# Optimization experiments

Hardware: AMD Instinct MI355X
Metric: run time of the kernel (lower is better)

Reference implementation:

```python
import jax, jax.numpy as jnp
import numpy as np

K = 5        # kernel_size per dim
DIM = 3      # pseudo-coordinate dim
KTOT = K ** DIM   # 125 kernel weight matrices
S = 2 ** DIM      # 8 basis products for degree-1 open B-spline
KNN = 3


def spline_basis(ea):
    """Degree-1 open B-spline basis. ea: [E, DIM] in [0,1).
    Returns basis [E, S] and kernel weight indices wi [E, S]."""
    v = ea * (K - 1)
    b = jnp.floor(v)
    f = v - b                      # fractional part, grads flow here
    bi = b.astype(jnp.int32)
    bases, idxs = [], []
    for c in range(S):             # static loop over 2^DIM corner combos
        bs = jnp.ones(ea.shape[0], ea.dtype)
        wi = jnp.zeros(ea.shape[0], jnp.int32)
        for d in range(DIM):
            bit = (c >> d) & 1
            bs = bs * (f[:, d] if bit else 1.0 - f[:, d])
            wi = wi + jnp.clip(bi[:, d] + bit, 0, K - 1) * (K ** d)
        bases.append(bs)
        idxs.append(wi)
    return jnp.stack(bases, 1), jnp.stack(idxs, 1)


def spline_conv(x, src, dst, basis, wi, W, Wroot, bias):
    """SplineConv with aggr='mean', root weight and bias (PyG defaults)."""
    N, Cin = x.shape
    E = src.shape[0]
    xs = x[src]                                   # [E, Cin] gather
    vals = xs[:, None, :] * basis[:, :, None]     # [E, S, Cin]
    seg = (dst[:, None] * KTOT + wi).reshape(-1)  # bucket by (dst node, kernel)
    A = jax.ops.segment_sum(vals.reshape(-1, Cin), seg,
                            num_segments=N * KTOT).reshape(N, KTOT, Cin)
    out = jnp.einsum('nki,kio->no', A, W)         # apply kernel bank once
    deg = jax.ops.segment_sum(jnp.ones(E, x.dtype), dst, num_segments=N)
    out = out / jnp.maximum(deg, 1.0)[:, None]    # mean aggregation
    return out + x @ Wroot + bias


def knn_interpolate(x, pos_x, pos_y, batch_x, batch_y, k):
    """PyG knn_interpolate: inverse-squared-distance weighted k-NN average."""
    off = 1e5  # separate batches in coordinate space
    px = pos_x + batch_x[:, None].astype(pos_x.dtype) * off
    py = pos_y + batch_y[:, None].astype(pos_y.dtype) * off
    d2 = (jnp.sum(py ** 2, 1)[:, None] + jnp.sum(px ** 2, 1)[None, :]
          - 2.0 * (py @ px.T))                    # [Ny, Nx]
    negd, idx = jax.lax.top_k(-d2, k)             # k nearest
    w = 1.0 / jnp.maximum(-negd, 1e-16)           # [Ny, k]
    return (w[:, :, None] * x[idx]).sum(1) / w.sum(1)[:, None]


def setup_inputs() -> dict:
    key = jax.random.key(0)
    ks = jax.random.split(key, 12)
    N, E, Ny, C = 8192, 131072, 16384, 64
    return {
        'x': jax.random.normal(ks[0], (N, C), jnp.float32),
        'edge_index': jax.random.randint(ks[1], (2, E), 0, N, jnp.int32),
        'edge_attr': jax.random.uniform(ks[2], (E, DIM), jnp.float32),
        'pos_x': jax.random.normal(ks[3], (N, 3), jnp.float32),
        'batch_x': jnp.zeros((N,), jnp.int32),
        'pos_y': jax.random.normal(ks[4], (Ny, 3), jnp.float32),
        'batch_y': jnp.zeros((Ny,), jnp.int32),
        'Wa': jax.random.normal(ks[5], (KTOT, C, C), jnp.float32) * 0.05,
        'roota': jax.random.normal(ks[6], (C, C), jnp.float32) * 0.05,
        'biasa': jnp.zeros((C,), jnp.float32),
        'Wb': jax.random.normal(ks[7], (KTOT, C, C), jnp.float32) * 0.05,
        'rootb': jax.random.normal(ks[8], (C, C), jnp.float32) * 0.05,
        'biasb': jnp.zeros((C,), jnp.float32),
    }


def reference(x, edge_index, edge_attr, pos_x, batch_x, pos_y, batch_y,
              Wa, roota, biasa, Wb, rootb, biasb):
    src, dst = edge_index[0], edge_index[1]
    basis, wi = spline_basis(edge_attr)
    h = jax.nn.elu(spline_conv(x, src, dst, basis, wi, Wa, roota, biasa))
    h = jax.nn.elu(spline_conv(h, src, dst, basis, wi, Wb, rootb, biasb))
    return knn_interpolate(h, pos_x, pos_y, batch_x, batch_y, KNN)
```

## Files before the change

### kernel.cpp

```cpp
#include <hip/hip_runtime.h>
#include <hip/hip_bf16.h>
#include <math.h>

#define CDIV(a,b) (((a)+(b)-1)/(b))
#define WPCV 8
#define KCH 32

typedef __attribute__((ext_vector_type(8))) short bf16x8;
typedef __attribute__((ext_vector_type(4))) float f32x4;

__device__ __forceinline__ float elu_f(float x){ return x > 0.f ? x : expm1f(x); }
__device__ __forceinline__ unsigned short f2bf(float x){
    __hip_bfloat16 h = __float2bfloat16(x);
    union { __hip_bfloat16 b; unsigned short u; } cv; cv.b = h; return cv.u;
}
__device__ __forceinline__ float bf2f(unsigned short u){
    unsigned int ui = ((unsigned int)u) << 16;
    union { unsigned int u; float f; } cv; cv.u = ui; return cv.f;
}

__global__ void k_basis_px(const float* __restrict__ ea, const int* __restrict__ dst,
                        float* __restrict__ basis, int* __restrict__ cellid,
                        int* __restrict__ cellcnt, int* __restrict__ deg,
                        int* __restrict__ rank, int E, int EB, int PB,
                        const float* __restrict__ posx, const int* __restrict__ bx,
                        float4* __restrict__ px4, int N,
                        const float* __restrict__ x, unsigned short* __restrict__ xbf)
{
    const int tid = threadIdx.x;
    const int bid = blockIdx.x;
    if (bid >= EB) {
        int r = bid - EB;
        if (r < PB) {
            int n = r*256 + tid;
            if (n < N) {
                float off = (float)bx[n] * 1e5f;
                float a = posx[n*3+0]+off, b = posx[n*3+1]+off, c = posx[n*3+2]+off;
                px4[n] = make_float4(a, b, c, a*a + b*b + c*c);
            }
        } else {
            int i = (r - PB)*256 + tid;
            if (i < N*8) {
                const float4* xs = (const float4*)x + (size_t)i*2;
                float4 a4 = xs[0], b4 = xs[1];
                bf16x8 v;
                v[0]=(short)f2bf(a4.x); v[1]=(short)f2bf(a4.y);
                v[2]=(short)f2bf(a4.z); v[3]=(short)f2bf(a4.w);
                v[4]=(short)f2bf(b4.x); v[5]=(short)f2bf(b4.y);
                v[6]=(short)f2bf(b4.z); v[7]=(short)f2bf(b4.w);
                *(bf16x8*)(xbf + (size_t)i*8) = v;
            }
        }
        return;
    }
    __shared__ int hist[64];
    if (tid < 64) hist[tid] = 0;
    __syncthreads();
    int e = bid * 256 + tid;
    if (e < E) {
        float f[3]; int bi[3];
        #pragma unroll
        for (int d = 0; d < 3; d++) {
            float v = ea[e*3+d] * 4.f;
            float b = floorf(v);
            f[d] = v - b;
            int bb = (int)b; bb = bb < 0 ? 0 : (bb > 3 ? 3 : bb);
            bi[d] = bb;
        }
        int cell = bi[0] + 4*bi[1] + 16*bi[2];
        cellid[e] = cell;
        atomicAdd(&hist[cell], 1);
        rank[e] = atomicAdd(deg + dst[e], 1);
        float bs[8];
        #pragma unroll
        for (int c = 0; c < 8; c++) {
            float b = 1.f;
            #pragma unroll
            for (int d = 0; d < 3; d++)
                b *= ((c>>d)&1) ? f[d] : (1.f - f[d]);
            bs[c] = b;
        }
        float4* bw = (float4*)(basis + (size_t)e*8);
        bw[0] = make_float4(bs[0],bs[1],bs[2],bs[3]);
        bw[1] = make_float4(bs[4],bs[5],bs[6],bs[7]);
    }
    __syncthreads();
    if (tid < 64 && hist[tid]) atomicAdd(cellcnt + tid, hist[tid]);
}

__global__ __launch_bounds__(1024) void k_degscan(const int* __restrict__ deg,
                        int* __restrict__ csr, float* __restrict__ invdeg, int N,
                        const int* __restrict__ cellcnt, int* __restrict__ cellstart,
                        int* __restrict__ cellfill)
{
    __shared__ int buf[2][1024];
    const int t = threadIdx.x;
    if (t < 64) {
        int v = cellcnt[t];
        int s = v;
        #pragma unroll
        for (int off = 1; off < 64; off <<= 1) {
            int o = __shfl_up(s, off, 64);
            if (t >= off) s += o;
        }
        cellstart[t] = s - v; cellfill[t] = s - v;
        if (t == 63) cellstart[64] = s;
    }
    const int base = t*8;
    int loc[8]; int s = 0;
    #pragma unroll
    for (int j = 0; j < 8; j++) {
        loc[j] = s;
        int d = (base+j < N) ? deg[base+j] : 0;
        if (base+j < N) invdeg[base+j] = 1.f / fmaxf((float)d, 1.f);
        s += d;
    }
    buf[0][t] = s; __syncthreads();
    int pb = 0;
    for (int off = 1; off < 1024; off <<= 1) {
        int v = buf[pb][t];
        if (t >= off) v += buf[pb][t-off];
        buf[pb^1][t] = v; __syncthreads(); pb ^= 1;
    }
    int excl = buf[pb][t] - s;
    #pragma unroll
    for (int j = 0; j < 8; j++)
        if (base+j < N) csr[base+j] = excl + loc[j];
    if (t == 0) csr[N] = buf[pb][1023];
}

__global__ __launch_bounds__(256) void k_pack(
    const int* __restrict__ cellid, int* __restrict__ fill, int* __restrict__ elist,
    const int* __restrict__ dst, const int* __restrict__ rank,
    const int* __restrict__ csr, int* __restrict__ dstpos, int E, int SB,
    const float* __restrict__ Wa, const float* __restrict__ Wb,
    unsigned short* __restrict__ WTa, unsigned short* __restrict__ WTb)
{
    __shared__ float shbuf[64*65];
    const int tid = threadIdx.x;
    const int bid = blockIdx.x;
    if (bid < SB) {
        int* hist = (int*)shbuf;
        int* bas  = hist + 64;
        if (tid < 64) hist[tid] = 0;
        __syncthreads();
        int e = bid * 256 + tid;
        int cell = 0, loc = 0;
        bool act = e < E;
        if (act) { cell = cellid[e]; loc = atomicAdd(&hist[cell], 1); }
        __syncthreads();
        if (tid < 64) bas[tid] = hist[tid] ? atomicAdd(fill + tid, hist[tid]) : 0;
        __syncthreads();
        if (act) elist[bas[cell] + loc] = e;
    } else if (bid < 2*SB) {
        int e = (bid - SB) * 256 + tid;
        if (e < E) dstpos[e] = csr[dst[e]] + rank[e];
    } else {
        int b = bid - 2*SB;
        float (*ws65)[65] = (float(*)[65])shbuf;
        const float* Wsrc = (b < 125) ? (Wa + (size_t)b*4096) : (Wb + (size_t)(b-125)*4096);
        unsigned short* Wdst = (b < 125) ? (WTa + (size_t)b*4096) : (WTb + (size_t)(b-125)*4096);
        #pragma unroll
        for (int j = 0; j < 16; j++) {
            int idx = j*256 + tid;
            ws65[idx>>6][idx&63] = Wsrc[idx];
        }
        __syncthreads();
        #pragma unroll
        for (int j = 0; j < 16; j++) {
            int idx = j*256 + tid;
            int o = idx>>6, i = idx&63;
            Wdst[idx] = f2bf(ws65[i][o]);
        }
    }
}

__global__ __launch_bounds__(256) void k_conv(
    const unsigned short* __restrict__ xin, const unsigned short* __restrict__ WT,
    const int* __restrict__ elist, const int* __restrict__ cellstart,
    const float* __restrict__ basis, const int* __restrict__ src,
    const int* __restrict__ dstpos, unsigned short* __restrict__ ye)
{
    __shared__ unsigned short wt[8][64][64];
    __shared__ unsigned short xb[64][64];
    __shared__ float bts[8][64];
    __shared__ int dpos[64];

    const int cell = blockIdx.x / WPCV;
    const int sub  = blockIdx.x % WPCV;
    const int tid  = threadIdx.x;
    const int w    = tid >> 6;
    const int lane = tid & 63;
    const int eh   = w >> 1;
    const int oh   = w & 1;
    const int l15  = lane & 15;
    const int kgrp = lane >> 4;
    const int swz  = lane & 7;

    int kc[8];
    {
        int b0 = cell & 3, b1 = (cell >> 2) & 3, b2 = (cell >> 4) & 3;
        #pragma unroll
        for (int c = 0; c < 8; c++)
            kc[c] = (b0 + (c&1)) + 5*(b1 + ((c>>1)&1)) + 25*(b2 + ((c>>2)&1));
    }

    #pragma unroll
    for (int j = 0; j < 16; j++) {
        int cj  = j >> 1;
        int off = ((j & 1) << 8) + tid;
        int row = off >> 3, colc = off & 7;
        bf16x8 v = ((const bf16x8*)(WT + (size_t)kc[cj]*4096))[off];
        *(bf16x8*)&wt[cj][row][(colc ^ (row & 7)) << 3] = v;
    }

    const int s0 = cellstart[cell], s1 = cellstart[cell+1];
    const int se = tid >> 2, sm = tid & 3;

    for (int base = s0 + sub*64; base < s1; base += WPCV*64) {
        int ne = s1 - base; ne = ne > 64 ? 64 : ne;
        __syncthreads();
        int c0 = (sm*2)     ^ (se & 7);
        int c1 = (sm*2 + 1) ^ (se & 7);
        if (se < ne) {
            int eid = elist[base + se];
            int sn  = src[eid];
            const bf16x8* xr = (const bf16x8*)(xin + (size_t)sn*64);
            bf16x8 v0 = xr[sm*2], v1 = xr[sm*2+1];
            *(bf16x8*)&xb[se][c0 << 3] = v0;
            *(bf16x8*)&xb[se][c1 << 3] = v1;
            if (sm == 0) {
                const float4* br = (const float4*)(basis + (size_t)eid*8);
                float4 bA = br[0], bB = br[1];
                bts[0][se]=bA.x; bts[1][se]=bA.y; bts[2][se]=bA.z; bts[3][se]=bA.w;
                bts[4][se]=bB.x; bts[5][se]=bB.y; bts[6][se]=bB.z; bts[7][se]=bB.w;
                dpos[se] = dstpos[eid];
            }
        } else {
            bf16x8 z = {0,0,0,0,0,0,0,0};
            *(bf16x8*)&xb[se][c0 << 3] = z;
            *(bf16x8*)&xb[se][c1 << 3] = z;
            if (sm == 0) dpos[se] = -1;
        }
        __syncthreads();

        bf16x8 a[2][2];
        #pragma unroll
        for (int me = 0; me < 2; me++) {
            int arow = eh*32 + me*16 + l15;
            #pragma unroll
            for (int kh = 0; kh < 2; kh++)
                a[me][kh] = *(const bf16x8*)&xb[arow][((kh*4 + kgrp) ^ swz) << 3];
        }

        f32x4 y[2][2] = {{{0,0,0,0},{0,0,0,0}},{{0,0,0,0},{0,0,0,0}}};
        #pragma unroll
        for (int c = 0; c < 8; c++) {
            float4 bv[2];
            bv[0] = *(const float4*)&bts[c][eh*32 +      (kgrp << 2)];
            bv[1] = *(const float4*)&bts[c][eh*32 + 16 + (kgrp << 2)];
            bf16x8 bfr[2][2];
            #pragma unroll
            for (int nb = 0; nb < 2; nb++) {
                int brow = oh*32 + nb*16 + l15;
                #pragma unroll
                for (int kh = 0; kh < 2; kh++)
                    bfr[nb][kh] = *(const bf16x8*)&wt[c][brow][((kh*4 + kgrp) ^ swz) << 3];
            }
            #pragma unroll
            for (int me = 0; me < 2; me++) {
                #pragma unroll
                for (int nb = 0; nb < 2; nb++) {
                    f32x4 t = {0.f, 0.f, 0.f, 0.f};
                    t = __builtin_amdgcn_mfma_f32_16x16x32_bf16(a[me][0], bfr[nb][0], t, 0, 0, 0);
                    t = __builtin_amdgcn_mfma_f32_16x16x32_bf16(a[me][1], bfr[nb][1], t, 0, 0, 0);
                    y[me][nb][0] = fmaf(bv[me].x, t[0], y[me][nb][0]);
                    y[me][nb][1] = fmaf(bv[me].y, t[1], y[me][nb][1]);
                    y[me][nb][2] = fmaf(bv[me].z, t[2], y[me][nb][2]);
                    y[me][nb][3] = fmaf(bv[me].w, t[3], y[me][nb][3]);
                }
            }
        }
        #pragma unroll
        for (int me = 0; me < 2; me++) {
            #pragma unroll
            for (int r = 0; r < 4; r++) {
                int el = eh*32 + me*16 + (kgrp << 2) + r;
                int dp = dpos[el];
                if (dp >= 0) {
                    unsigned short* yp = ye + (size_t)dp*64 + oh*32 + l15;
                    yp[0]  = f2bf(y[me][0][r]);
                    yp[16] = f2bf(y[me][1][r]);
                }
            }
        }
    }
}

__global__ __launch_bounds__(256) void k_gather(
    const unsigned short* __restrict__ ye, const int* __restrict__ csr,
    const unsigned short* __restrict__ xin, const float* __restrict__ root,
    const float* __restrict__ bias, const float* __restrict__ invdeg,
    unsigned short* __restrict__ hout, int N)
{
    __shared__ float sh[4][64];
    const int w = threadIdx.x >> 6, lane = threadIdx.x & 63;
    const int n = blockIdx.x*4 + w;
    if (n >= N) return;
    const int s0 = csr[n], s1 = csr[n+1];
    const int j8 = lane >> 3, c8 = lane & 7;
    float acc[8] = {};
    for (int base = s0; base < s1; base += 8) {
        int ei = base + j8;
        if (ei < s1) {
            bf16x8 v = *(const bf16x8*)(ye + (size_t)ei*64 + c8*8);
            #pragma unroll
            for (int k = 0; k < 8; k++)
                acc[k] += bf2f((unsigned short)v[k]);
        }
    }
    #pragma unroll
    for (int m = 8; m <= 32; m <<= 1) {
        #pragma unroll
        for (int k = 0; k < 8; k++)
            acc[k] += __shfl_xor(acc[k], m, 64);
    }
    if (j8 == 0) {
        #pragma unroll
        for (int k = 0; k < 8; k++) sh[w][c8*8+k] = acc[k];
    }
    float aggr = sh[w][lane];
    float av = aggr * invdeg[n];
    float xv = bf2f(xin[(size_t)n*64 + lane]);
    float rt = bias[lane];
    #pragma unroll 8
    for (int i = 0; i < 64; i++)
        rt = fmaf(__shfl(xv, i, 64), root[i*64 + lane], rt);
    hout[(size_t)n*64 + lane] = f2bf(elu_f(av + rt));
}

__global__ __launch_bounds__(256) void k_knn_part(
    const float4* __restrict__ px4, const float* __restrict__ posy,
    const int* __restrict__ by, float* __restrict__ pd, int* __restrict__ pi,
    int N, int Ny)
{
    const int qb  = (blockIdx.x / KCH) * 256;
    const int ch  = blockIdx.x % KCH;
    const int NC  = N / KCH;
    const int tid = threadIdx.x;
    const int q = qb + tid;
    float off = (float)by[q] * 1e5f;
    float qa = posy[q*3+0]+off, qbv = posy[q*3+1]+off, qc = posy[q*3+2]+off;
    float sy = qa*qa + qbv*qbv + qc*qc;
    float qa2 = -2.f*qa, qb2 = -2.f*qbv, qc2 = -2.f*qc;

    const float4* __restrict__ pts = px4 + (size_t)ch * NC;
    const int gbase = ch * NC;

    float d0 = 3.4e38f, d1 = 3.4e38f, d2s = 3.4e38f;
    int   i0 = 0x7fffffff, i1 = 0x7fffffff, i2 = 0x7fffffff;
    #pragma unroll 16
    for (int p = 0; p < NC; p++) {
        float4 pt = pts[p];
        float u  = fmaf(qa2, pt.x, fmaf(qb2, pt.y, fmaf(qc2, pt.z, sy + pt.w)));
        int   gi = gbase + p;
        bool c0 = u < d0, c1 = u < d1, c2 = u < d2s;
        float nd0 = fminf(d0, u);
        float nd1 = __builtin_amdgcn_fmed3f(d0, u, d1);
        float nd2 = __builtin_amdgcn_fmed3f(u, d1, d2s);
        i2 = c1 ? i1 : (c2 ? gi : i2);
        i1 = c0 ? i0 : (c1 ? gi : i1);
        i0 = c0 ? gi : i0;
        d0 = nd0; d1 = nd1; d2s = nd2;
    }
    size_t ob = ((size_t)ch*Ny + q)*3;
    pd[ob+0]=d0; pd[ob+1]=d1; pd[ob+2]=d2s;
    pi[ob+0]=i0; pi[ob+1]=i1; pi[ob+2]=i2;
}

__global__ __launch_bounds__(256) void k_knn_merge(
    const float* __restrict__ pd, const int* __restrict__ pi,
    const unsigned short* __restrict__ h2, float* __restrict__ out, int Ny)
{
    const int w = threadIdx.x >> 6, lane = threadIdx.x & 63;
    const int q = blockIdx.x*4 + w;
    float a0 = 3.4e38f, a1 = 3.4e38f, a2 = 3.4e38f;
    int   b0 = 0x7fffffff, b1 = 0x7fffffff, b2 = 0x7fffffff;
    if (lane < KCH) {
        size_t base = ((size_t)lane*Ny + q)*3;
        a0 = pd[base+0]; a1 = pd[base+1]; a2 = pd[base+2];
        b0 = pi[base+0]; b1 = pi[base+1]; b2 = pi[base+2];
    }
    float rd[3]; int ri[3];
    #pragma unroll
    for (int j = 0; j < 3; j++) {
        float md = a0; int mi = b0;
        #pragma unroll
        for (int s = 1; s < 64; s <<= 1) {
            float od = __shfl_xor(md, s, 64);
            int   oi = __shfl_xor(mi, s, 64);
            if (od < md || (od == md && oi < mi)) { md = od; mi = oi; }
        }
        rd[j] = md; ri[j] = mi;
        if (b0 == mi) { a0=a1; b0=b1; a1=a2; b1=b2; a2=3.4e38f; b2=0x7fffffff; }
    }
    float w0 = 1.f/fmaxf(rd[0], 1e-16f);
    float w1 = 1.f/fmaxf(rd[1], 1e-16f);
    float w2 = 1.f/fmaxf(rd[2], 1e-16f);
    float ws = w0 + w1 + w2;
    float v = w0*bf2f(h2[(size_t)ri[0]*64+lane]) + w1*bf2f(h2[(size_t)ri[1]*64+lane])
            + w2*bf2f(h2[(size_t)ri[2]*64+lane]);
    out[(size_t)q*64+lane] = v / ws;
}

extern "C" void kernel_launch(void* const* d_in, const int* in_sizes, int n_in,
                              void* d_out, int out_size, void* d_ws, size_t ws_size,
                              hipStream_t stream)
{
    const float* x     = (const float*)d_in[0];
    const int*   ei    = (const int*)d_in[1];
    const float* ea    = (const float*)d_in[2];
    const float* posx  = (const float*)d_in[3];
    const int*   bx    = (const int*)d_in[4];
    const float* posy  = (const float*)d_in[5];
    const int*   by    = (const int*)d_in[6];
    const float* Wa    = (const float*)d_in[7];
    const float* roota = (const float*)d_in[8];
    const float* biasa = (const float*)d_in[9];
    const float* Wb    = (const float*)d_in[10];
    const float* rootb = (const float*)d_in[11];
    const float* biasb = (const float*)d_in[12];

    const int N  = in_sizes[0] / 64;
    const int E  = in_sizes[1] / 2;
    const int Ny = in_sizes[5] / 3;
    const int* srcp = ei;
    const int* dstp = ei + E;

    char* ws = (char*)d_ws;
    size_t off = 0;
    auto alloc = [&](size_t bytes) { void* p = ws + off; off += (bytes + 255) & ~255ull; return p; };
    float*  basis    = (float*)alloc((size_t)E*8*4);
    int*    cellid   = (int*)  alloc((size_t)E*4);
    int*    rank     = (int*)  alloc((size_t)E*4);
    int*    elist    = (int*)  alloc((size_t)E*4);
    int*    dstpos   = (int*)  alloc((size_t)E*4);
    int*    deg      = (int*)  alloc((size_t)N*4);
    int*    cellcnt  = (int*)  alloc(64*4);
    int*    csr      = (int*)  alloc((size_t)(N+1)*4);
    float*  invdeg   = (float*)alloc((size_t)N*4);
    int*    cellstart= (int*)  alloc(65*4);
    int*    cellfill = (int*)  alloc(64*4);
    unsigned short* xbf = (unsigned short*)alloc((size_t)N*64*2);
    unsigned short* h1  = (unsigned short*)alloc((size_t)N*64*2);
    unsigned short* h2  = (unsigned short*)alloc((size_t)N*64*2);
    float4* px4      = (float4*)alloc((size_t)N*16);
    unsigned short* WTa = (unsigned short*)alloc((size_t)125*4096*2);
    unsigned short* WTb = (unsigned short*)alloc((size_t)125*4096*2);
    unsigned short* ye  = (unsigned short*)alloc((size_t)E*64*2);
    float* pd = (float*)ye;
    int*   pi = (int*)((char*)ye + ((size_t)8<<20));
    (void)ws_size; (void)n_in; (void)out_size;

    const int EB = CDIV(E,256);
    const int PB = CDIV(N,256);
    const int XB = CDIV(N*8,256);

    hipMemsetAsync(deg, 0, (size_t)N*4 + 256, stream);

    k_basis_px<<<EB+PB+XB, 256, 0, stream>>>(ea, dstp, basis, cellid, cellcnt, deg, rank,
                                             E, EB, PB, posx, bx, px4, N, x, xbf);
    k_degscan <<<1, 1024, 0, stream>>>(deg, csr, invdeg, N, cellcnt, cellstart, cellfill);
    k_pack    <<<2*EB + 250, 256, 0, stream>>>(cellid, cellfill, elist, dstp, rank,
                                               csr, dstpos, E, EB, Wa, Wb, WTa, WTb);

    k_conv  <<<64*WPCV, 256, 0, stream>>>(xbf, WTa, elist, cellstart, basis, srcp, dstpos, ye);
    k_gather<<<CDIV(N,4), 256, 0, stream>>>(ye, csr, xbf, roota, biasa, invdeg, h1, N);

    k_conv  <<<64*WPCV, 256, 0, stream>>>(h1, WTb, elist, cellstart, basis, srcp, dstpos, ye);
    k_gather<<<CDIV(N,4), 256, 0, stream>>>(ye, csr, h1, rootb, biasb, invdeg, h2, N);

    k_knn_part <<<(Ny/256)*KCH, 256, 0, stream>>>(px4, posy, by, pd, pi, N, Ny);
    k_knn_merge<<<Ny/4, 256, 0, stream>>>(pd, pi, h2, (float*)d_out, Ny);
}
```

Measured before the change: 176.8 us.

## Fuse kNN search and merge into one wave-per-8-queries kernel with ballot filtering

Replaces the chunked kNN partial-top3 kernel plus merge kernel with a single kernel in which each wavefront handles 8 queries. The 64 lanes scan 64 points at a time, and a ballot against the current third-best distance lets the wave insert only the few candidates that can improve the list, done serially. This removes the partial-result round trip through memory and the second launch, and it avoids per-point top-3 maintenance in every thread. The trade-offs are lower parallelism (Ny/8 waves each scanning all N points), data-dependent divergent loops, and a requirement that N be a multiple of 64.

```diff
diff --git a/kernel.cpp b/kernel.cpp
--- a/kernel.cpp
+++ b/kernel.cpp
@@ -4,7 +4,7 @@
 
 #define CDIV(a,b) (((a)+(b)-1)/(b))
 #define WPCV 8
-#define KCH 32
+#define QPW 8
 
 typedef __attribute__((ext_vector_type(8))) short bf16x8;
 typedef __attribute__((ext_vector_type(4))) float f32x4;
@@ -339,78 +339,92 @@
     hout[(size_t)n*64 + lane] = f2bf(elu_f(av + rt));
 }
 
-__global__ __launch_bounds__(256) void k_knn_part(
+__global__ __launch_bounds__(256) void k_knn(
     const float4* __restrict__ px4, const float* __restrict__ posy,
-    const int* __restrict__ by, float* __restrict__ pd, int* __restrict__ pi,
-    int N, int Ny)
-{
-    const int qb  = (blockIdx.x / KCH) * 256;
-    const int ch  = blockIdx.x % KCH;
-    const int NC  = N / KCH;
-    const int tid = threadIdx.x;
-    const int q = qb + tid;
-    float off = (float)by[q] * 1e5f;
-    float qa = posy[q*3+0]+off, qbv = posy[q*3+1]+off, qc = posy[q*3+2]+off;
-    float sy = qa*qa + qbv*qbv + qc*qc;
-    float qa2 = -2.f*qa, qb2 = -2.f*qbv, qc2 = -2.f*qc;
-
-    const float4* __restrict__ pts = px4 + (size_t)ch * NC;
-    const int gbase = ch * NC;
-
-    float d0 = 3.4e38f, d1 = 3.4e38f, d2s = 3.4e38f;
-    int   i0 = 0x7fffffff, i1 = 0x7fffffff, i2 = 0x7fffffff;
-    #pragma unroll 16
-    for (int p = 0; p < NC; p++) {
-        float4 pt = pts[p];
-        float u  = fmaf(qa2, pt.x, fmaf(qb2, pt.y, fmaf(qc2, pt.z, sy + pt.w)));
-        int   gi = gbase + p;
-        bool c0 = u < d0, c1 = u < d1, c2 = u < d2s;
-        float nd0 = fminf(d0, u);
-        float nd1 = __builtin_amdgcn_fmed3f(d0, u, d1);
-        float nd2 = __builtin_amdgcn_fmed3f(u, d1, d2s);
-        i2 = c1 ? i1 : (c2 ? gi : i2);
-        i1 = c0 ? i0 : (c1 ? gi : i1);
-        i0 = c0 ? gi : i0;
-        d0 = nd0; d1 = nd1; d2s = nd2;
-    }
-    size_t ob = ((size_t)ch*Ny + q)*3;
-    pd[ob+0]=d0; pd[ob+1]=d1; pd[ob+2]=d2s;
-    pi[ob+0]=i0; pi[ob+1]=i1; pi[ob+2]=i2;
-}
-
-__global__ __launch_bounds__(256) void k_knn_merge(
-    const float* __restrict__ pd, const int* __restrict__ pi,
-    const unsigned short* __restrict__ h2, float* __restrict__ out, int Ny)
-{
-    const int w = threadIdx.x >> 6, lane = threadIdx.x & 63;
-    const int q = blockIdx.x*4 + w;
-    float a0 = 3.4e38f, a1 = 3.4e38f, a2 = 3.4e38f;
-    int   b0 = 0x7fffffff, b1 = 0x7fffffff, b2 = 0x7fffffff;
-    if (lane < KCH) {
-        size_t base = ((size_t)lane*Ny + q)*3;
-        a0 = pd[base+0]; a1 = pd[base+1]; a2 = pd[base+2];
-        b0 = pi[base+0]; b1 = pi[base+1]; b2 = pi[base+2];
-    }
-    float rd[3]; int ri[3];
-    #pragma unroll
-    for (int j = 0; j < 3; j++) {
-        float md = a0; int mi = b0;
-        #pragma unroll
-        for (int s = 1; s < 64; s <<= 1) {
-            float od = __shfl_xor(md, s, 64);
-            int   oi = __shfl_xor(mi, s, 64);
-            if (od < md || (od == md && oi < mi)) { md = od; mi = oi; }
-        }
-        rd[j] = md; ri[j] = mi;
-        if (b0 == mi) { a0=a1; b0=b1; a1=a2; b1=b2; a2=3.4e38f; b2=0x7fffffff; }
-    }
-    float w0 = 1.f/fmaxf(rd[0], 1e-16f);
-    float w1 = 1.f/fmaxf(rd[1], 1e-16f);
-    float w2 = 1.f/fmaxf(rd[2], 1e-16f);
-    float ws = w0 + w1 + w2;
-    float v = w0*bf2f(h2[(size_t)ri[0]*64+lane]) + w1*bf2f(h2[(size_t)ri[1]*64+lane])
-            + w2*bf2f(h2[(size_t)ri[2]*64+lane]);
-    out[(size_t)q*64+lane] = v / ws;
+    const int* __restrict__ by, const unsigned short* __restrict__ h2,
+    float* __restrict__ out, int N, int Ny)
+{
+    const int wid  = blockIdx.x*4 + (threadIdx.x >> 6);
+    const int lane = threadIdx.x & 63;
+    const int qbase = wid * QPW;
+
+    int ql = qbase + (lane & (QPW-1));
+    float offv = (float)by[ql] * 1e5f;
+    float qa = posy[ql*3+0]+offv, qb = posy[ql*3+1]+offv, qc = posy[ql*3+2]+offv;
+    float sy_l  = qa*qa + qb*qb + qc*qc;
+    float a2_l = -2.f*qa, b2_l = -2.f*qb, c2_l = -2.f*qc;
+
+    float SY[QPW], A2[QPW], B2[QPW], C2[QPW];
+    float d0[QPW], d1[QPW], d2s[QPW];
+    int   i0[QPW], i1[QPW], i2[QPW];
+    #pragma unroll
+    for (int g = 0; g < QPW; g++) {
+        SY[g] = __shfl(sy_l, g);
+        A2[g] = __shfl(a2_l, g);
+        B2[g] = __shfl(b2_l, g);
+        C2[g] = __shfl(c2_l, g);
+    }
+
+    {
+        float4 p0 = px4[lane];
+        #pragma unroll
+        for (int g = 0; g < QPW; g++) {
+            float u = fmaf(A2[g], p0.x, fmaf(B2[g], p0.y, fmaf(C2[g], p0.z, SY[g] + p0.w)));
+            float uu = u;
+            #pragma unroll
+            for (int j = 0; j < 3; j++) {
+                float md = uu; int mi = lane;
+                #pragma unroll
+                for (int s = 1; s < 64; s <<= 1) {
+                    float od = __shfl_xor(md, s, 64);
+                    int   oi = __shfl_xor(mi, s, 64);
+                    if (od < md || (od == md && oi < mi)) { md = od; mi = oi; }
+                }
+                if (j == 0) { d0[g] = md; i0[g] = mi; }
+                else if (j == 1) { d1[g] = md; i1[g] = mi; }
+                else { d2s[g] = md; i2[g] = mi; }
+                if (lane == mi) uu = 3.4e38f;
+            }
+        }
+    }
+
+    const int nb = N >> 6;
+    float4 cur = px4[64 + lane];
+    for (int b = 1; b < nb; b++) {
+        float4 nxt;
+        if (b + 1 < nb) nxt = px4[(size_t)((b+1) << 6) + lane];
+        const int gb = b << 6;
+        #pragma unroll
+        for (int g = 0; g < QPW; g++) {
+            float u = fmaf(A2[g], cur.x, fmaf(B2[g], cur.y, fmaf(C2[g], cur.z, SY[g] + cur.w)));
+            unsigned long long m = __ballot(u < d2s[g]);
+            while (m) {
+                int l = __builtin_ctzll(m);
+                m &= m - 1;
+                float uc = __shfl(u, l);
+                int   ic = gb + l;
+                bool c0 = uc < d0[g], c1 = uc < d1[g], c2 = uc < d2s[g];
+                float Md  = c0 ? d0[g] : uc;  int Mi  = c0 ? i0[g] : ic;
+                float Md1 = c1 ? d1[g] : Md;  int Mi1 = c1 ? i1[g] : Mi;
+                d2s[g] = c2 ? Md1 : d2s[g];   i2[g] = c2 ? Mi1 : i2[g];
+                d1[g]  = c1 ? Md  : d1[g];    i1[g] = c1 ? Mi  : i1[g];
+                d0[g]  = c0 ? uc  : d0[g];    i0[g] = c0 ? ic  : i0[g];
+            }
+        }
+        cur = nxt;
+    }
+
+    #pragma unroll
+    for (int g = 0; g < QPW; g++) {
+        float w0 = 1.f/fmaxf(d0[g],  1e-16f);
+        float w1 = 1.f/fmaxf(d1[g],  1e-16f);
+        float w2 = 1.f/fmaxf(d2s[g], 1e-16f);
+        float wsum = w0 + w1 + w2;
+        float v = w0*bf2f(h2[(size_t)i0[g]*64 + lane])
+                + w1*bf2f(h2[(size_t)i1[g]*64 + lane])
+                + w2*bf2f(h2[(size_t)i2[g]*64 + lane]);
+        out[(size_t)(qbase + g)*64 + lane] = v / wsum;
+    }
 }
 
 extern "C" void kernel_launch(void* const* d_in, const int* in_sizes, int n_in,
@@ -458,8 +472,6 @@
     unsigned short* WTa = (unsigned short*)alloc((size_t)125*4096*2);
     unsigned short* WTb = (unsigned short*)alloc((size_t)125*4096*2);
     unsigned short* ye  = (unsigned short*)alloc((size_t)E*64*2);
-    float* pd = (float*)ye;
-    int*   pi = (int*)((char*)ye + ((size_t)8<<20));
     (void)ws_size; (void)n_in; (void)out_size;
 
     const int EB = CDIV(E,256);
@@ -480,6 +492,5 @@
     k_conv  <<<64*WPCV, 256, 0, stream>>>(h1, WTb, elist, cellstart, basis, srcp, dstpos, ye);
     k_gather<<<CDIV(N,4), 256, 0, stream>>>(ye, csr, h1, rootb, biasb, invdeg, h2, N);
 
-    k_knn_part <<<(Ny/256)*KCH, 256, 0, stream>>>(px4, posy, by, pd, pi, N, Ny);
-    k_knn_merge<<<Ny/4, 256, 0, stream>>>(pd, pi, h2, (float*)d_out, Ny);
-}
+    k_knn<<<Ny/(QPW*4), 256, 0, stream>>>(px4, posy, by, h2, (float*)d_out, N, Ny);
+}
```

After: 200.5 us. 1.13x slower.

## Fuse kNN partial search into the two gather kernels as extra blocks

Applied to the files above, without the earlier changes.

Removes the standalone kNN partial-distance kernel and splits its 32 point chunks across the two gather launches, 16 chunks each, as extra leading blocks. The kNN search depends only on positions, so it can overlap with the memory-bound gather work and one launch is dropped. The partial-result buffers now get their own allocations instead of aliasing the ye buffer, which the gather still reads concurrently. The cost is more blocks per gather launch and heavier blocks that may delay gather completion.

```diff
diff --git a/kernel.cpp b/kernel.cpp
--- a/kernel.cpp
+++ b/kernel.cpp
@@ -297,15 +297,56 @@
     }
 }
 
-__global__ __launch_bounds__(256) void k_gather(
+__global__ __launch_bounds__(256) void k_gather_knn(
     const unsigned short* __restrict__ ye, const int* __restrict__ csr,
     const unsigned short* __restrict__ xin, const float* __restrict__ root,
     const float* __restrict__ bias, const float* __restrict__ invdeg,
-    unsigned short* __restrict__ hout, int N)
+    unsigned short* __restrict__ hout, int N, int KB,
+    const float4* __restrict__ px4, const float* __restrict__ posy,
+    const int* __restrict__ by, float* __restrict__ pd, int* __restrict__ pi,
+    int Npts, int Ny, int chbase)
 {
     __shared__ float sh[4][64];
-    const int w = threadIdx.x >> 6, lane = threadIdx.x & 63;
-    const int n = blockIdx.x*4 + w;
+    const int bid = blockIdx.x;
+    const int tid = threadIdx.x;
+
+    if (bid < KB) {
+        const int qb  = (bid / 16) * 256;
+        const int ch  = chbase + (bid % 16);
+        const int NC  = Npts / KCH;
+        const int q = qb + tid;
+        float off = (float)by[q] * 1e5f;
+        float qa = posy[q*3+0]+off, qbv = posy[q*3+1]+off, qc = posy[q*3+2]+off;
+        float sy = qa*qa + qbv*qbv + qc*qc;
+        float qa2 = -2.f*qa, qb2 = -2.f*qbv, qc2 = -2.f*qc;
+
+        const float4* __restrict__ pts = px4 + (size_t)ch * NC;
+        const int gbase = ch * NC;
+
+        float d0 = 3.4e38f, d1 = 3.4e38f, d2s = 3.4e38f;
+        int   i0 = 0x7fffffff, i1 = 0x7fffffff, i2 = 0x7fffffff;
+        #pragma unroll 16
+        for (int p = 0; p < NC; p++) {
+            float4 pt = pts[p];
+            float u  = fmaf(qa2, pt.x, fmaf(qb2, pt.y, fmaf(qc2, pt.z, sy + pt.w)));
+            int   gi = gbase + p;
+            bool c0 = u < d0, c1 = u < d1, c2 = u < d2s;
+            float nd0 = fminf(d0, u);
+            float nd1 = __builtin_amdgcn_fmed3f(d0, u, d1);
+            float nd2 = __builtin_amdgcn_fmed3f(u, d1, d2s);
+            i2 = c1 ? i1 : (c2 ? gi : i2);
+            i1 = c0 ? i0 : (c1 ? gi : i1);
+            i0 = c0 ? gi : i0;
+            d0 = nd0; d1 = nd1; d2s = nd2;
+        }
+        size_t ob = ((size_t)ch*Ny + q)*3;
+        pd[ob+0]=d0; pd[ob+1]=d1; pd[ob+2]=d2s;
+        pi[ob+0]=i0; pi[ob+1]=i1; pi[ob+2]=i2;
+        return;
+    }
+
+    const int w = tid >> 6, lane = tid & 63;
+    const int n = (bid - KB)*4 + w;
     if (n >= N) return;
     const int s0 = csr[n], s1 = csr[n+1];
     const int j8 = lane >> 3, c8 = lane & 7;
@@ -337,45 +378,6 @@
     for (int i = 0; i < 64; i++)
         rt = fmaf(__shfl(xv, i, 64), root[i*64 + lane], rt);
     hout[(size_t)n*64 + lane] = f2bf(elu_f(av + rt));
-}
-
-__global__ __launch_bounds__(256) void k_knn_part(
-    const float4* __restrict__ px4, const float* __restrict__ posy,
-    const int* __restrict__ by, float* __restrict__ pd, int* __restrict__ pi,
-    int N, int Ny)
-{
-    const int qb  = (blockIdx.x / KCH) * 256;
-    const int ch  = blockIdx.x % KCH;
-    const int NC  = N / KCH;
-    const int tid = threadIdx.x;
-    const int q = qb + tid;
-    float off = (float)by[q] * 1e5f;
-    float qa = posy[q*3+0]+off, qbv = posy[q*3+1]+off, qc = posy[q*3+2]+off;
-    float sy = qa*qa + qbv*qbv + qc*qc;
-    float qa2 = -2.f*qa, qb2 = -2.f*qbv, qc2 = -2.f*qc;
-
-    const float4* __restrict__ pts = px4 + (size_t)ch * NC;
-    const int gbase = ch * NC;
-
-    float d0 = 3.4e38f, d1 = 3.4e38f, d2s = 3.4e38f;
-    int   i0 = 0x7fffffff, i1 = 0x7fffffff, i2 = 0x7fffffff;
-    #pragma unroll 16
-    for (int p = 0; p < NC; p++) {
-        float4 pt = pts[p];
-        float u  = fmaf(qa2, pt.x, fmaf(qb2, pt.y, fmaf(qc2, pt.z, sy + pt.w)));
-        int   gi = gbase + p;
-        bool c0 = u < d0, c1 = u < d1, c2 = u < d2s;
-        float nd0 = fminf(d0, u);
-        float nd1 = __builtin_amdgcn_fmed3f(d0, u, d1);
-        float nd2 = __builtin_amdgcn_fmed3f(u, d1, d2s);
-        i2 = c1 ? i1 : (c2 ? gi : i2);
-        i1 = c0 ? i0 : (c1 ? gi : i1);
-        i0 = c0 ? gi : i0;
-        d0 = nd0; d1 = nd1; d2s = nd2;
-    }
-    size_t ob = ((size_t)ch*Ny + q)*3;
-    pd[ob+0]=d0; pd[ob+1]=d1; pd[ob+2]=d2s;
-    pi[ob+0]=i0; pi[ob+1]=i1; pi[ob+2]=i2;
 }
 
 __global__ __launch_bounds__(256) void k_knn_merge(
@@ -458,13 +460,15 @@
     unsigned short* WTa = (unsigned short*)alloc((size_t)125*4096*2);
     unsigned short* WTb = (unsigned short*)alloc((size_t)125*4096*2);
     unsigned short* ye  = (unsigned short*)alloc((size_t)E*64*2);
-    float* pd = (float*)ye;
-    int*   pi = (int*)((char*)ye + ((size_t)8<<20));
+    float* pd = (float*)alloc((size_t)Ny*KCH*3*4);
+    int*   pi = (int*)  alloc((size_t)Ny*KCH*3*4);
     (void)ws_size; (void)n_in; (void)out_size;
 
     const int EB = CDIV(E,256);
     const int PB = CDIV(N,256);
     const int XB = CDIV(N*8,256);
+    const int GB = CDIV(N,4);
+    const int KB = (Ny/256)*16;
 
     hipMemsetAsync(deg, 0, (size_t)N*4 + 256, stream);
 
@@ -474,12 +478,13 @@
     k_pack    <<<2*EB + 250, 256, 0, stream>>>(cellid, cellfill, elist, dstp, rank,
                                                csr, dstpos, E, EB, Wa, Wb, WTa, WTb);
 
-    k_conv  <<<64*WPCV, 256, 0, stream>>>(xbf, WTa, elist, cellstart, basis, srcp, dstpos, ye);
-    k_gather<<<CDIV(N,4), 256, 0, stream>>>(ye, csr, xbf, roota, biasa, invdeg, h1, N);
-
-    k_conv  <<<64*WPCV, 256, 0, stream>>>(h1, WTb, elist, cellstart, basis, srcp, dstpos, ye);
-    k_gather<<<CDIV(N,4), 256, 0, stream>>>(ye, csr, h1, rootb, biasb, invdeg, h2, N);
-
-    k_knn_part <<<(Ny/256)*KCH, 256, 0, stream>>>(px4, posy, by, pd, pi, N, Ny);
+    k_conv      <<<64*WPCV, 256, 0, stream>>>(xbf, WTa, elist, cellstart, basis, srcp, dstpos, ye);
+    k_gather_knn<<<KB+GB, 256, 0, stream>>>(ye, csr, xbf, roota, biasa, invdeg, h1, N, KB,
+                                            px4, posy, by, pd, pi, N, Ny, 0);
+
+    k_conv      <<<64*WPCV, 256, 0, stream>>>(h1, WTb, elist, cellstart, basis, srcp, dstpos, ye);
+    k_gather_knn<<<KB+GB, 256, 0, stream>>>(ye, csr, h1, rootb, biasb, invdeg, h2, N, KB,
+                                            px4, posy, by, pd, pi, N, Ny, 16);
+
     k_knn_merge<<<Ny/4, 256, 0, stream>>>(pd, pi, h2, (float*)d_out, Ny);
 }
```

New measurement: 165.2 us. -6.6%, faster.
